# Optimization experiments

Hardware: AMD Instinct MI355X
Metric: run time of the kernel (lower is better)

Reference implementation:

```python
import jax, jax.numpy as jnp
from jax import lax
import numpy as np

NUM_CLASSES = 80
STRIDES = (8, 16, 32)
CONF_THRE = 0.01
NMS_THRE = 0.65
TOPK = 500  # fixed pre-NMS candidate cap (jit-compatible stand-in for dynamic conf filter)


def setup_inputs() -> dict:
    key = jax.random.key(0)
    k8, k16, k32 = jax.random.split(key, 3)
    B, C = 8, 5 + NUM_CLASSES
    return {
        "out8": jax.random.normal(k8, (B, C, 160, 160), dtype=jnp.float32),
        "out16": jax.random.normal(k16, (B, C, 80, 80), dtype=jnp.float32),
        "out32": jax.random.normal(k32, (B, C, 40, 40), dtype=jnp.float32),
    }


def _decode_level(x, stride):
    # x: [B, C, H, W] -> decoded [B, H*W, C]
    B, C, H, W = x.shape
    x = x.reshape(B, C, H * W).transpose(0, 2, 1)  # [B, HW, C]
    yv, xv = jnp.meshgrid(jnp.arange(H), jnp.arange(W), indexing="ij")
    grid = jnp.stack([xv, yv], axis=-1).reshape(1, H * W, 2).astype(x.dtype)
    s = jnp.asarray(stride, x.dtype)
    xy = (x[..., 0:2] + grid) * s
    wh = jnp.exp(x[..., 2:4]) * s
    obj = jax.nn.sigmoid(x[..., 4:5])
    cls = jax.nn.sigmoid(x[..., 5:])
    return jnp.concatenate([xy, wh, obj, cls], axis=-1)


def _iou_one_vs_all(box, boxes):
    # box: [4] xyxy, boxes: [K,4] xyxy
    x1 = jnp.maximum(box[0], boxes[:, 0])
    y1 = jnp.maximum(box[1], boxes[:, 1])
    x2 = jnp.minimum(box[2], boxes[:, 2])
    y2 = jnp.minimum(box[3], boxes[:, 3])
    inter = jnp.maximum(x2 - x1, 0.0) * jnp.maximum(y2 - y1, 0.0)
    a1 = jnp.maximum(box[2] - box[0], 0.0) * jnp.maximum(box[3] - box[1], 0.0)
    a2 = jnp.maximum(boxes[:, 2] - boxes[:, 0], 0.0) * jnp.maximum(boxes[:, 3] - boxes[:, 1], 0.0)
    return inter / (a1 + a2 - inter + 1e-9)


def _nms_keep(boxes, valid, iou_thr):
    # boxes are pre-sorted by descending score; returns bool keep mask [K]
    K = boxes.shape[0]
    idx = jnp.arange(K)

    def body(i, state):
        keep, suppressed = state
        cur_ok = jnp.logical_not(suppressed[i])
        keep = keep.at[i].set(cur_ok)
        iou = _iou_one_vs_all(boxes[i], boxes)
        suppressed = suppressed | ((iou > iou_thr) & cur_ok & (idx > i))
        return keep, suppressed

    keep, _ = lax.fori_loop(0, K, body, (jnp.zeros(K, bool), jnp.logical_not(valid)))
    return keep


def _post_process_image(pred):
    # pred: [N, 5+num_classes] decoded, boxes already xyxy
    cls_scores = pred[:, 5:5 + NUM_CLASSES]
    class_conf = jnp.max(cls_scores, axis=1)
    class_pred = jnp.argmax(cls_scores, axis=1)
    obj = pred[:, 4]
    total = obj * class_conf  # NMS score, same as torchvision call
    masked = jnp.where(total >= CONF_THRE, total, -1.0)
    top_sc, top_i = lax.top_k(masked, TOPK)  # sorted descending
    boxes = pred[top_i, :4]
    obj_k = obj[top_i]
    cc_k = class_conf[top_i]
    lab_k = class_pred[top_i]
    valid = top_sc >= CONF_THRE
    # class-aware (batched) NMS via per-class coordinate offset, as torchvision does
    max_c = jnp.max(jnp.where(valid[:, None], boxes, 0.0)) + 1.0
    boxes_off = boxes + (lab_k.astype(boxes.dtype) * max_c)[:, None]
    keep = _nms_keep(boxes_off, valid, NMS_THRE)
    det = jnp.concatenate(
        [boxes, obj_k[:, None], cc_k[:, None], lab_k.astype(boxes.dtype)[:, None]], axis=1
    )  # [K, 7] = (x1,y1,x2,y2,obj,class_conf,class_id)
    return det * keep[:, None].astype(det.dtype)


def reference(out8, out16, out32):
    levels = [(out8, 8), (out16, 16), (out32, 32)]
    pred = jnp.concatenate([_decode_level(x, s) for x, s in levels], axis=1)  # [B, N, C]
    # cxcywh -> xyxy corners
    cx, cy, w, h = pred[..., 0], pred[..., 1], pred[..., 2], pred[..., 3]
    corners = jnp.stack([cx - w / 2, cy - h / 2, cx + w / 2, cy + h / 2], axis=-1)
    pred = jnp.concatenate([corners, pred[..., 4:]], axis=-1)
    return jax.vmap(_post_process_image)(pred)  # [B, TOPK, 7], zero-padded
```

## Files before the change

kernel.cpp:

```cpp
#include <hip/hip_runtime.h>

#define NPI    33600
#define KTOP   500
#define CAP    1024
#define KEY001 0xBC23D70Au
#define NGRP   1024
#define NIMG   8

__device__ __forceinline__ float sigmoidf_(float x) {
  return 1.0f / (1.0f + expf(-x));
}
__device__ __forceinline__ unsigned fkey(float f) {
  unsigned u = __float_as_uint(f);
  return (u & 0x80000000u) ? ~u : (u | 0x80000000u);
}

__global__ __launch_bounds__(256) void k_decode(
    const float* __restrict__ p8, const float* __restrict__ p16,
    const float* __restrict__ p32,
    unsigned* __restrict__ keys, float* __restrict__ dets,
    unsigned* __restrict__ hist2)
{
  const int b = blockIdx.y;
  const int t = blockIdx.x * 256 + threadIdx.x;
  const int a = t * 4;
  __shared__ unsigned lh[NGRP];
  for (int i = threadIdx.x; i < NGRP; i += 256) lh[i] = 0;
  __syncthreads();

  if (a < NPI) {
    const float* lvl; int j, W, HW, S;
    if (a < 25600)      { lvl = p8;  j = a;         W = 160; HW = 25600; S = 8;  }
    else if (a < 32000) { lvl = p16; j = a - 25600; W = 80;  HW = 6400;  S = 16; }
    else                { lvl = p32; j = a - 32000; W = 40;  HW = 1600;  S = 32; }
    const float* base = lvl + (size_t)b * 85 * HW + j;
    float4 t0 = *(const float4*)(base);
    float4 t1 = *(const float4*)(base + (size_t)1 * HW);
    float4 t2 = *(const float4*)(base + (size_t)2 * HW);
    float4 t3 = *(const float4*)(base + (size_t)3 * HW);
    float4 t4 = *(const float4*)(base + (size_t)4 * HW);
    float cc[4] = {-1.0f, -1.0f, -1.0f, -1.0f};
    int   lab[4] = {0, 0, 0, 0};
    #pragma unroll
    for (int c0 = 0; c0 < 80; c0 += 8) {
      float4 r[8];
      #pragma unroll
      for (int u = 0; u < 8; ++u)
        r[u] = *(const float4*)(base + (size_t)(5 + c0 + u) * HW);
      #pragma unroll
      for (int u = 0; u < 8; ++u) {
        float s;
        s = sigmoidf_(r[u].x); if (s > cc[0]) { cc[0] = s; lab[0] = c0 + u; }
        s = sigmoidf_(r[u].y); if (s > cc[1]) { cc[1] = s; lab[1] = c0 + u; }
        s = sigmoidf_(r[u].z); if (s > cc[2]) { cc[2] = s; lab[2] = c0 + u; }
        s = sigmoidf_(r[u].w); if (s > cc[3]) { cc[3] = s; lab[3] = c0 + u; }
      }
    }
    float e0[4] = {t0.x, t0.y, t0.z, t0.w};
    float e1[4] = {t1.x, t1.y, t1.z, t1.w};
    float e2[4] = {t2.x, t2.y, t2.z, t2.w};
    float e3[4] = {t3.x, t3.y, t3.z, t3.w};
    float e4[4] = {t4.x, t4.y, t4.z, t4.w};
    unsigned k4[4];
    float dv[7][4];
    #pragma unroll
    for (int e = 0; e < 4; ++e) {
      float obj = sigmoidf_(e4[e]);
      float tot = obj * cc[e];
      k4[e] = fkey(tot >= 0.01f ? tot : -1.0f);
      int jj = j + e;
      int gy = jj / W, gx = jj - gy * W;
      float fs = (float)S;
      float cx = (e0[e] + (float)gx) * fs;
      float cy = (e1[e] + (float)gy) * fs;
      float w  = expf(e2[e]) * fs;
      float h  = expf(e3[e]) * fs;
      dv[0][e] = cx - 0.5f * w; dv[1][e] = cy - 0.5f * h;
      dv[2][e] = cx + 0.5f * w; dv[3][e] = cy + 0.5f * h;
      dv[4][e] = obj; dv[5][e] = cc[e]; dv[6][e] = (float)lab[e];
    }
    *(uint4*)(keys + (size_t)b * NPI + a) = make_uint4(k4[0], k4[1], k4[2], k4[3]);
    const size_t P  = (size_t)NIMG * NPI;
    const size_t pa = (size_t)b * NPI + a;
    #pragma unroll
    for (int c = 0; c < 7; ++c)
      *(float4*)(dets + (size_t)c * P + pa) =
          make_float4(dv[c][0], dv[c][1], dv[c][2], dv[c][3]);
    #pragma unroll
    for (int e = 0; e < 4; ++e) atomicAdd(&lh[k4[e] >> 22], 1u);
  }
  __syncthreads();
  unsigned* gb = hist2 + (size_t)b * NGRP;
  for (int i = threadIdx.x; i < NGRP; i += 256) {
    unsigned v = lh[i];
    if (v) atomicAdd(&gb[i], v);
  }
}

__global__ __launch_bounds__(1024) void k_post(
    const unsigned* __restrict__ hist2, const unsigned* __restrict__ keys,
    const float* __restrict__ dets, float* __restrict__ out)
{
  const int b    = blockIdx.x;
  const int tid  = threadIdx.x;
  const int lane = tid & 63;
  const int wave = tid >> 6;

  __shared__ unsigned lh[NGRP];
  __shared__ unsigned sh_sub[4096];
  __shared__ unsigned sh_c64[64];
  __shared__ unsigned sh_G, sh_Chi10, sh_T, sh_Chi, sh_nA, sh_nB;
  __shared__ unsigned long long sh_cand[CAP];
  __shared__ float sh_det[KTOP][7];
  __shared__ float sh_box[KTOP][4];
  __shared__ unsigned sh_mask[KTOP * 16];
  __shared__ unsigned sh_inval[16];
  __shared__ unsigned sh_keep[16];
  __shared__ unsigned sh_wcA[16], sh_wcB[16];
  __shared__ float sh_red[16];
  __shared__ float sh_maxc;

  lh[tid] = hist2[(size_t)b * NGRP + tid];
  for (int i = tid; i < 4096; i += 1024) sh_sub[i] = 0;
  __syncthreads();
  if (tid < 64) {
    unsigned s = 0;
    #pragma unroll
    for (int k = 0; k < 16; ++k) s += lh[tid * 16 + k];
    sh_c64[tid] = s;
  }
  __syncthreads();
  if (tid == 0) {
    unsigned cum = 0; int C = 0;
    for (int g = 63; g >= 0; --g) {
      unsigned v = sh_c64[g];
      if (cum + v >= KTOP) { C = g; break; }
      cum += v;
    }
    int G = C * 16; unsigned chi = cum;
    for (int g = C * 16 + 15; g >= C * 16; --g) {
      unsigned v = lh[g];
      if (chi + v >= KTOP) { G = g; break; }
      chi += v;
    }
    sh_G = (unsigned)G; sh_Chi10 = chi;
    sh_nA = 0; sh_nB = 0;
  }
  __syncthreads();
  const unsigned G = sh_G;
  const unsigned* kb = keys + (size_t)b * NPI;

  for (int i = tid; i < NPI; i += 1024) {
    unsigned k = kb[i];
    if ((k >> 22) == G) atomicAdd(&sh_sub[(k >> 10) & 4095u], 1u);
  }
  __syncthreads();
  if (tid < 64) {
    unsigned s = 0;
    for (int k = 0; k < 64; ++k) s += sh_sub[tid * 64 + k];
    sh_c64[tid] = s;
  }
  __syncthreads();
  if (tid == 0) {
    unsigned c = sh_Chi10; int C2 = 0;
    for (int g = 63; g >= 0; --g) {
      unsigned v = sh_c64[g];
      if (c + v >= KTOP) { C2 = g; break; }
      c += v;
    }
    int T12 = C2 * 64;
    for (int t2 = C2 * 64 + 63; t2 >= C2 * 64; --t2) {
      unsigned v = sh_sub[t2];
      if (c + v >= KTOP) { T12 = t2; break; }
      c += v;
    }
    sh_T = (G << 12) | (unsigned)T12;
    sh_Chi = c;
  }
  __syncthreads();
  const unsigned T = sh_T, Chi = sh_Chi;
  const unsigned Bcap = CAP - Chi;

  for (int chunk = 0; chunk < 9; ++chunk) {
    int a0 = chunk * 4096 + tid * 4;
    unsigned kk[4]; bool iA[4], iB[4];
    bool act = (a0 < NPI);
    if (act) {
      uint4 kv = *(const uint4*)(kb + a0);
      kk[0] = kv.x; kk[1] = kv.y; kk[2] = kv.z; kk[3] = kv.w;
    } else { kk[0] = kk[1] = kk[2] = kk[3] = 0u; }
    #pragma unroll
    for (int e = 0; e < 4; ++e) {
      unsigned bin = kk[e] >> 10;
      iA[e] = act && (bin > T);
      iB[e] = act && (bin == T);
    }
    unsigned long long balA[4], balB[4];
    #pragma unroll
    for (int e = 0; e < 4; ++e) { balA[e] = __ballot(iA[e]); balB[e] = __ballot(iB[e]); }
    if (lane == 0) {
      unsigned sA = 0, sB = 0;
      #pragma unroll
      for (int e = 0; e < 4; ++e) { sA += (unsigned)__popcll(balA[e]); sB += (unsigned)__popcll(balB[e]); }
      sh_wcA[wave] = sA; sh_wcB[wave] = sB;
    }
    __syncthreads();
    unsigned pA = sh_nA, pB = sh_nB;
    for (int w2 = 0; w2 < wave; ++w2) { pA += sh_wcA[w2]; pB += sh_wcB[w2]; }
    unsigned long long lt = (1ULL << lane) - 1ULL;
    #pragma unroll
    for (int e = 0; e < 4; ++e) {
      pA += (unsigned)__popcll(balA[e] & lt);
      pB += (unsigned)__popcll(balB[e] & lt);
    }
    #pragma unroll
    for (int e = 0; e < 4; ++e) {
      unsigned long long packed =
          ((unsigned long long)kk[e] << 32) |
          (unsigned long long)(0xFFFFFFFFu - (unsigned)(a0 + e));
      if (iA[e]) { sh_cand[pA] = packed; ++pA; }
      if (iB[e]) { if (pB < Bcap) sh_cand[CAP - 1 - pB] = packed; ++pB; }
    }
    __syncthreads();
    if (tid == 0) {
      unsigned sA = 0, sB = 0;
      for (int w2 = 0; w2 < 16; ++w2) { sA += sh_wcA[w2]; sB += sh_wcB[w2]; }
      sh_nA += sA; sh_nB += sB;
    }
    __syncthreads();
  }
  {
    const unsigned nA  = sh_nA;
    const unsigned nBk = (sh_nB < Bcap) ? sh_nB : Bcap;
    for (int s = (int)nA + tid; s < (int)(CAP - nBk); s += 1024) sh_cand[s] = 0ULL;
  }
  __syncthreads();

  for (unsigned kk2 = 2; kk2 <= CAP; kk2 <<= 1) {
    for (unsigned jj = kk2 >> 1; jj > 0; jj >>= 1) {
      unsigned i = (unsigned)tid, p = i ^ jj;
      if (p > i) {
        unsigned long long x = sh_cand[i], y = sh_cand[p];
        bool desc = ((i & kk2) == 0);
        if ((x < y) == desc) { sh_cand[i] = y; sh_cand[p] = x; }
      }
      __syncthreads();
    }
  }

  bool validk = false;
  float contrib = -INFINITY;
  if (tid < KTOP) {
    unsigned long long v = sh_cand[tid];
    unsigned keyk = (unsigned)(v >> 32);
    int a = (int)(0xFFFFFFFFu - (unsigned)(v & 0xFFFFFFFFull));
    if (a < 0) a = 0;
    const size_t P  = (size_t)NIMG * NPI;
    const size_t pa = (size_t)b * NPI + (size_t)a;
    float det[7];
    #pragma unroll
    for (int c = 0; c < 7; ++c) det[c] = dets[(size_t)c * P + pa];
    #pragma unroll
    for (int c = 0; c < 7; ++c) sh_det[tid][c] = det[c];
    validk = (keyk >= KEY001);
    float m4 = fmaxf(fmaxf(det[0], det[1]), fmaxf(det[2], det[3]));
    contrib = validk ? m4 : 0.0f;
  }
  float r = contrib;
  #pragma unroll
  for (int off = 32; off > 0; off >>= 1) r = fmaxf(r, __shfl_xor(r, off));
  if (lane == 0) sh_red[wave] = r;
  unsigned long long bv = __ballot((tid < KTOP) && !validk);
  if (wave < 8 && lane == 0) {
    sh_inval[wave * 2]     = (unsigned)(bv & 0xFFFFFFFFull);
    sh_inval[wave * 2 + 1] = (unsigned)(bv >> 32);
  }
  __syncthreads();
  if (tid == 0) {
    float m = -INFINITY;
    for (int w2 = 0; w2 < 16; ++w2) m = fmaxf(m, sh_red[w2]);
    sh_maxc = m + 1.0f;
  }
  __syncthreads();
  const float maxc = sh_maxc;
  if (tid < KTOP) {
    float offb = sh_det[tid][6] * maxc;
    #pragma unroll
    for (int d = 0; d < 4; ++d) sh_box[tid][d] = sh_det[tid][d] + offb;
  }
  __syncthreads();

  for (int task = tid; task < KTOP * 16; task += 1024) {
    int i = task % KTOP;
    int w = task / KTOP;
    int jbase = w * 32;
    unsigned bits = 0u;
    if (jbase + 31 > i) {
      float ix1 = sh_box[i][0], iy1 = sh_box[i][1], ix2 = sh_box[i][2], iy2 = sh_box[i][3];
      float a1 = fmaxf(ix2 - ix1, 0.0f) * fmaxf(iy2 - iy1, 0.0f);
      #pragma unroll 4
      for (int jj = 0; jj < 32; ++jj) {
        int j = jbase + jj;
        if (j < KTOP && j > i) {
          float jx1 = sh_box[j][0], jy1 = sh_box[j][1];
          float jx2 = sh_box[j][2], jy2 = sh_box[j][3];
          float iw = fminf(ix2, jx2) - fmaxf(ix1, jx1);
          float ih = fminf(iy2, jy2) - fmaxf(iy1, jy1);
          float inter = fmaxf(iw, 0.0f) * fmaxf(ih, 0.0f);
          float a2 = fmaxf(jx2 - jx1, 0.0f) * fmaxf(jy2 - jy1, 0.0f);
          if (inter > 0.65f * (a1 + a2 - inter + 1e-9f)) bits |= (1u << jj);
        }
      }
    }
    sh_mask[i * 16 + w] = bits;
  }
  __syncthreads();

  if (tid < 64) {
    unsigned sup   = (lane < 16) ? sh_inval[lane] : 0u;
    unsigned keepw = 0u;
    unsigned cur = (unsigned)__builtin_amdgcn_readlane((int)sup, 0);
    unsigned mA = (lane < 16) ? sh_mask[0 * 16 + lane] : 0u;
    unsigned mB = (lane < 16) ? sh_mask[1 * 16 + lane] : 0u;
    for (int i = 0; i < KTOP; i += 2) {
      bool ok = ((cur >> (i & 31)) & 1u) == 0u;
      if (ok) {
        sup |= mA;
        if (lane == (i >> 5)) keepw |= (1u << (i & 31));
      }
      cur = (unsigned)__builtin_amdgcn_readlane((int)sup, (i + 1) >> 5);
      mA = (lane < 16 && (i + 2) < KTOP) ? sh_mask[(i + 2) * 16 + lane] : 0u;
      bool ok2 = ((cur >> ((i + 1) & 31)) & 1u) == 0u;
      if (ok2) {
        sup |= mB;
        if (lane == ((i + 1) >> 5)) keepw |= (1u << ((i + 1) & 31));
      }
      cur = (unsigned)__builtin_amdgcn_readlane((int)sup, (i + 2) >> 5);
      mB = (lane < 16 && (i + 3) < KTOP) ? sh_mask[(i + 3) * 16 + lane] : 0u;
    }
    if (lane < 16) sh_keep[lane] = keepw;
  }
  __syncthreads();

  for (int x = tid; x < KTOP * 7; x += 1024) {
    int k = x / 7, c = x - k * 7;
    float keepf = ((sh_keep[k >> 5] >> (k & 31)) & 1u) ? 1.0f : 0.0f;
    out[(size_t)b * (KTOP * 7) + x] = sh_det[k][c] * keepf;
  }
}

extern "C" void kernel_launch(void* const* d_in, const int* in_sizes, int n_in,
                              void* d_out, int out_size, void* d_ws, size_t ws_size,
                              hipStream_t stream) {
  const float* p8  = (const float*)d_in[0];
  const float* p16 = (const float*)d_in[1];
  const float* p32 = (const float*)d_in[2];
  float* out = (float*)d_out;
  unsigned* hist2 = (unsigned*)d_ws;
  unsigned* keys  = hist2 + (size_t)NIMG * NGRP;
  float*    dets  = (float*)(keys + (size_t)NIMG * NPI);

  hipMemsetAsync(hist2, 0, (size_t)NIMG * NGRP * 4, stream);
  k_decode<<<dim3(33, NIMG), 256, 0, stream>>>(p8, p16, p32, keys, dets, hist2);
  k_post<<<dim3(NIMG), 1024, 0, stream>>>(hist2, keys, dets, out);
}
```

Baseline: 250.0 us.

## Split post-processing into select, IoU and NMS kernels; retile decode per level

The decode kernel now uses 128-thread blocks that each stay within one pyramid level, and it loads 16 class channels per batch. The single 8-block post kernel is split into three kernels. A selection kernel does two-pass per-wave candidate compaction, which removes the per-chunk block barriers. An IoU kernel spreads the pairwise mask computation over 16x8 blocks using an SoA box layout with precomputed areas. An NMS kernel reads the mask back into padded shared memory. The goal is more parallelism for the IoU stage and fewer barriers during selection, in exchange for two extra launches and global round-trips of the mask and detections.

```diff
diff --git a/kernel.cpp b/kernel.cpp
--- a/kernel.cpp
+++ b/kernel.cpp
@@ -6,6 +6,7 @@
 #define KEY001 0xBC23D70Au
 #define NGRP   1024
 #define NIMG   8
+#define GPW    525
 
 __device__ __forceinline__ float sigmoidf_(float x) {
   return 1.0f / (1.0f + expf(-x));
@@ -15,25 +16,26 @@
   return (u & 0x80000000u) ? ~u : (u | 0x80000000u);
 }
 
-__global__ __launch_bounds__(256) void k_decode(
+__global__ __launch_bounds__(128) void k_decode(
     const float* __restrict__ p8, const float* __restrict__ p16,
     const float* __restrict__ p32,
     unsigned* __restrict__ keys, float* __restrict__ dets,
     unsigned* __restrict__ hist2)
 {
-  const int b = blockIdx.y;
-  const int t = blockIdx.x * 256 + threadIdx.x;
-  const int a = t * 4;
+  const int b  = blockIdx.y;
+  const int tx = blockIdx.x;
+  const float* lvl; int HW, W, S, j0, abase;
+  if (tx < 50)      { lvl = p8;  HW = 25600; W = 160; S = 8;  j0 = tx * 512;        abase = 0; }
+  else if (tx < 63) { lvl = p16; HW = 6400;  W = 80;  S = 16; j0 = (tx - 50) * 512; abase = 25600; }
+  else              { lvl = p32; HW = 1600;  W = 40;  S = 32; j0 = (tx - 63) * 512; abase = 32000; }
   __shared__ unsigned lh[NGRP];
-  for (int i = threadIdx.x; i < NGRP; i += 256) lh[i] = 0;
-  __syncthreads();
-
-  if (a < NPI) {
-    const float* lvl; int j, W, HW, S;
-    if (a < 25600)      { lvl = p8;  j = a;         W = 160; HW = 25600; S = 8;  }
-    else if (a < 32000) { lvl = p16; j = a - 25600; W = 80;  HW = 6400;  S = 16; }
-    else                { lvl = p32; j = a - 32000; W = 40;  HW = 1600;  S = 32; }
-    const float* base = lvl + (size_t)b * 85 * HW + j;
+  for (int i = threadIdx.x; i < NGRP; i += 128) lh[i] = 0;
+  __syncthreads();
+
+  const int e = j0 + 4 * threadIdx.x;
+  const bool act = (e < HW);
+  if (act) {
+    const float* base = lvl + (size_t)b * 85 * HW + e;
     float4 t0 = *(const float4*)(base);
     float4 t1 = *(const float4*)(base + (size_t)1 * HW);
     float4 t2 = *(const float4*)(base + (size_t)2 * HW);
@@ -41,19 +43,18 @@
     float4 t4 = *(const float4*)(base + (size_t)4 * HW);
     float cc[4] = {-1.0f, -1.0f, -1.0f, -1.0f};
     int   lab[4] = {0, 0, 0, 0};
-    #pragma unroll
-    for (int c0 = 0; c0 < 80; c0 += 8) {
-      float4 r[8];
+    for (int c0 = 5; c0 < 85; c0 += 16) {
+      float4 r[16];
       #pragma unroll
-      for (int u = 0; u < 8; ++u)
-        r[u] = *(const float4*)(base + (size_t)(5 + c0 + u) * HW);
+      for (int u = 0; u < 16; ++u)
+        r[u] = *(const float4*)(base + (size_t)(c0 + u) * HW);
       #pragma unroll
-      for (int u = 0; u < 8; ++u) {
+      for (int u = 0; u < 16; ++u) {
         float s;
-        s = sigmoidf_(r[u].x); if (s > cc[0]) { cc[0] = s; lab[0] = c0 + u; }
-        s = sigmoidf_(r[u].y); if (s > cc[1]) { cc[1] = s; lab[1] = c0 + u; }
-        s = sigmoidf_(r[u].z); if (s > cc[2]) { cc[2] = s; lab[2] = c0 + u; }
-        s = sigmoidf_(r[u].w); if (s > cc[3]) { cc[3] = s; lab[3] = c0 + u; }
+        s = sigmoidf_(r[u].x); if (s > cc[0]) { cc[0] = s; lab[0] = c0 + u - 5; }
+        s = sigmoidf_(r[u].y); if (s > cc[1]) { cc[1] = s; lab[1] = c0 + u - 5; }
+        s = sigmoidf_(r[u].z); if (s > cc[2]) { cc[2] = s; lab[2] = c0 + u - 5; }
+        s = sigmoidf_(r[u].w); if (s > cc[3]) { cc[3] = s; lab[3] = c0 + u - 5; }
       }
     }
     float e0[4] = {t0.x, t0.y, t0.z, t0.w};
@@ -64,21 +65,22 @@
     unsigned k4[4];
     float dv[7][4];
     #pragma unroll
-    for (int e = 0; e < 4; ++e) {
-      float obj = sigmoidf_(e4[e]);
-      float tot = obj * cc[e];
-      k4[e] = fkey(tot >= 0.01f ? tot : -1.0f);
-      int jj = j + e;
+    for (int q = 0; q < 4; ++q) {
+      float obj = sigmoidf_(e4[q]);
+      float tot = obj * cc[q];
+      k4[q] = fkey(tot >= 0.01f ? tot : -1.0f);
+      int jj = e + q;
       int gy = jj / W, gx = jj - gy * W;
       float fs = (float)S;
-      float cx = (e0[e] + (float)gx) * fs;
-      float cy = (e1[e] + (float)gy) * fs;
-      float w  = expf(e2[e]) * fs;
-      float h  = expf(e3[e]) * fs;
-      dv[0][e] = cx - 0.5f * w; dv[1][e] = cy - 0.5f * h;
-      dv[2][e] = cx + 0.5f * w; dv[3][e] = cy + 0.5f * h;
-      dv[4][e] = obj; dv[5][e] = cc[e]; dv[6][e] = (float)lab[e];
-    }
+      float cx = (e0[q] + (float)gx) * fs;
+      float cy = (e1[q] + (float)gy) * fs;
+      float w  = expf(e2[q]) * fs;
+      float h  = expf(e3[q]) * fs;
+      dv[0][q] = cx - 0.5f * w; dv[1][q] = cy - 0.5f * h;
+      dv[2][q] = cx + 0.5f * w; dv[3][q] = cy + 0.5f * h;
+      dv[4][q] = obj; dv[5][q] = cc[q]; dv[6][q] = (float)lab[q];
+    }
+    const int a = abase + e;
     *(uint4*)(keys + (size_t)b * NPI + a) = make_uint4(k4[0], k4[1], k4[2], k4[3]);
     const size_t P  = (size_t)NIMG * NPI;
     const size_t pa = (size_t)b * NPI + a;
@@ -87,19 +89,21 @@
       *(float4*)(dets + (size_t)c * P + pa) =
           make_float4(dv[c][0], dv[c][1], dv[c][2], dv[c][3]);
     #pragma unroll
-    for (int e = 0; e < 4; ++e) atomicAdd(&lh[k4[e] >> 22], 1u);
+    for (int q = 0; q < 4; ++q) atomicAdd(&lh[k4[q] >> 22], 1u);
   }
   __syncthreads();
   unsigned* gb = hist2 + (size_t)b * NGRP;
-  for (int i = threadIdx.x; i < NGRP; i += 256) {
+  for (int i = threadIdx.x; i < NGRP; i += 128) {
     unsigned v = lh[i];
     if (v) atomicAdd(&gb[i], v);
   }
 }
 
-__global__ __launch_bounds__(1024) void k_post(
+__global__ __launch_bounds__(1024) void k_select(
     const unsigned* __restrict__ hist2, const unsigned* __restrict__ keys,
-    const float* __restrict__ dets, float* __restrict__ out)
+    const float* __restrict__ dets,
+    float* __restrict__ topdet, float* __restrict__ soa,
+    unsigned* __restrict__ invalg)
 {
   const int b    = blockIdx.x;
   const int tid  = threadIdx.x;
@@ -109,13 +113,10 @@
   __shared__ unsigned lh[NGRP];
   __shared__ unsigned sh_sub[4096];
   __shared__ unsigned sh_c64[64];
-  __shared__ unsigned sh_G, sh_Chi10, sh_T, sh_Chi, sh_nA, sh_nB;
-  __shared__ unsigned long long sh_cand[CAP];
+  __shared__ unsigned sh_G, sh_T;
+  __shared__ __align__(16) unsigned long long sh_cand[CAP];
   __shared__ float sh_det[KTOP][7];
-  __shared__ float sh_box[KTOP][4];
-  __shared__ unsigned sh_mask[KTOP * 16];
   __shared__ unsigned sh_inval[16];
-  __shared__ unsigned sh_keep[16];
   __shared__ unsigned sh_wcA[16], sh_wcB[16];
   __shared__ float sh_red[16];
   __shared__ float sh_maxc;
@@ -143,17 +144,22 @@
       if (chi + v >= KTOP) { G = g; break; }
       chi += v;
     }
-    sh_G = (unsigned)G; sh_Chi10 = chi;
-    sh_nA = 0; sh_nB = 0;
+    sh_G = (unsigned)G;
+    sh_c64[0] = chi;
   }
   __syncthreads();
   const unsigned G = sh_G;
   const unsigned* kb = keys + (size_t)b * NPI;
 
-  for (int i = tid; i < NPI; i += 1024) {
-    unsigned k = kb[i];
-    if ((k >> 22) == G) atomicAdd(&sh_sub[(k >> 10) & 4095u], 1u);
-  }
+  for (int g = tid; g < NPI / 4; g += 1024) {
+    uint4 kv = ((const uint4*)kb)[g];
+    unsigned kk[4] = {kv.x, kv.y, kv.z, kv.w};
+    #pragma unroll
+    for (int q = 0; q < 4; ++q)
+      if ((kk[q] >> 22) == G) atomicAdd(&sh_sub[(kk[q] >> 10) & 4095u], 1u);
+  }
+  __syncthreads();
+  unsigned chi10 = sh_c64[0];
   __syncthreads();
   if (tid < 64) {
     unsigned s = 0;
@@ -162,7 +168,7 @@
   }
   __syncthreads();
   if (tid == 0) {
-    unsigned c = sh_Chi10; int C2 = 0;
+    unsigned c = chi10; int C2 = 0;
     for (int g = 63; g >= 0; --g) {
       unsigned v = sh_c64[g];
       if (c + v >= KTOP) { C2 = g; break; }
@@ -175,65 +181,74 @@
       c += v;
     }
     sh_T = (G << 12) | (unsigned)T12;
-    sh_Chi = c;
-  }
-  __syncthreads();
-  const unsigned T = sh_T, Chi = sh_Chi;
-  const unsigned Bcap = CAP - Chi;
-
-  for (int chunk = 0; chunk < 9; ++chunk) {
-    int a0 = chunk * 4096 + tid * 4;
-    unsigned kk[4]; bool iA[4], iB[4];
-    bool act = (a0 < NPI);
-    if (act) {
-      uint4 kv = *(const uint4*)(kb + a0);
-      kk[0] = kv.x; kk[1] = kv.y; kk[2] = kv.z; kk[3] = kv.w;
-    } else { kk[0] = kk[1] = kk[2] = kk[3] = 0u; }
-    #pragma unroll
-    for (int e = 0; e < 4; ++e) {
-      unsigned bin = kk[e] >> 10;
-      iA[e] = act && (bin > T);
-      iB[e] = act && (bin == T);
-    }
+  }
+  __syncthreads();
+  const unsigned T = sh_T;
+
+  unsigned runA = 0, runB = 0;
+  for (int it = 0; it < 9; ++it) {
+    int gl = it * 64 + lane;
+    bool act = (gl < GPW);
+    int g = wave * GPW + gl;
+    uint4 kv = act ? ((const uint4*)kb)[g] : make_uint4(0, 0, 0, 0);
+    unsigned kk[4] = {kv.x, kv.y, kv.z, kv.w};
+    #pragma unroll
+    for (int q = 0; q < 4; ++q) {
+      unsigned bin = kk[q] >> 10;
+      runA += (unsigned)__popcll(__ballot(act && (bin > T)));
+      runB += (unsigned)__popcll(__ballot(act && (bin == T)));
+    }
+  }
+  if (lane == 0) { sh_wcA[wave] = runA; sh_wcB[wave] = runB; }
+  __syncthreads();
+  unsigned pA = 0, pB = 0, nA = 0, nBtot = 0;
+  #pragma unroll
+  for (int w2 = 0; w2 < 16; ++w2) {
+    unsigned va = sh_wcA[w2], vb = sh_wcB[w2];
+    if (w2 < wave) { pA += va; pB += vb; }
+    nA += va; nBtot += vb;
+  }
+  const unsigned Bcap = CAP - nA;
+  const unsigned nBk  = (nBtot < Bcap) ? nBtot : Bcap;
+  const int nTot = (int)(nA + nBk);
+
+  for (int it = 0; it < 9; ++it) {
+    int gl = it * 64 + lane;
+    bool act = (gl < GPW);
+    int g = wave * GPW + gl;
+    uint4 kv = act ? ((const uint4*)kb)[g] : make_uint4(0, 0, 0, 0);
+    unsigned kk[4] = {kv.x, kv.y, kv.z, kv.w};
+    bool iA[4], iB[4];
     unsigned long long balA[4], balB[4];
     #pragma unroll
-    for (int e = 0; e < 4; ++e) { balA[e] = __ballot(iA[e]); balB[e] = __ballot(iB[e]); }
-    if (lane == 0) {
-      unsigned sA = 0, sB = 0;
-      #pragma unroll
-      for (int e = 0; e < 4; ++e) { sA += (unsigned)__popcll(balA[e]); sB += (unsigned)__popcll(balB[e]); }
-      sh_wcA[wave] = sA; sh_wcB[wave] = sB;
-    }
-    __syncthreads();
-    unsigned pA = sh_nA, pB = sh_nB;
-    for (int w2 = 0; w2 < wave; ++w2) { pA += sh_wcA[w2]; pB += sh_wcB[w2]; }
+    for (int q = 0; q < 4; ++q) {
+      unsigned bin = kk[q] >> 10;
+      iA[q] = act && (bin > T);
+      iB[q] = act && (bin == T);
+      balA[q] = __ballot(iA[q]);
+      balB[q] = __ballot(iB[q]);
+    }
     unsigned long long lt = (1ULL << lane) - 1ULL;
-    #pragma unroll
-    for (int e = 0; e < 4; ++e) {
-      pA += (unsigned)__popcll(balA[e] & lt);
-      pB += (unsigned)__popcll(balB[e] & lt);
-    }
-    #pragma unroll
-    for (int e = 0; e < 4; ++e) {
+    unsigned pAl = pA, pBl = pB;
+    #pragma unroll
+    for (int q = 0; q < 4; ++q) {
+      pAl += (unsigned)__popcll(balA[q] & lt);
+      pBl += (unsigned)__popcll(balB[q] & lt);
+    }
+    #pragma unroll
+    for (int q = 0; q < 4; ++q) {
+      int a0 = g * 4 + q;
       unsigned long long packed =
-          ((unsigned long long)kk[e] << 32) |
-          (unsigned long long)(0xFFFFFFFFu - (unsigned)(a0 + e));
-      if (iA[e]) { sh_cand[pA] = packed; ++pA; }
-      if (iB[e]) { if (pB < Bcap) sh_cand[CAP - 1 - pB] = packed; ++pB; }
-    }
-    __syncthreads();
-    if (tid == 0) {
-      unsigned sA = 0, sB = 0;
-      for (int w2 = 0; w2 < 16; ++w2) { sA += sh_wcA[w2]; sB += sh_wcB[w2]; }
-      sh_nA += sA; sh_nB += sB;
-    }
-    __syncthreads();
-  }
-  {
-    const unsigned nA  = sh_nA;
-    const unsigned nBk = (sh_nB < Bcap) ? sh_nB : Bcap;
-    for (int s = (int)nA + tid; s < (int)(CAP - nBk); s += 1024) sh_cand[s] = 0ULL;
-  }
+          ((unsigned long long)kk[q] << 32) |
+          (unsigned long long)(0xFFFFFFFFu - (unsigned)a0);
+      if (iA[q]) { sh_cand[pAl] = packed; ++pAl; }
+      if (iB[q]) { if (pBl < Bcap) sh_cand[nA + pBl] = packed; ++pBl; }
+      pA += (unsigned)__popcll(balA[q]);
+      pB += (unsigned)__popcll(balB[q]);
+    }
+  }
+  __syncthreads();
+  for (int s = nTot + tid; s < CAP; s += 1024) sh_cand[s] = 0ULL;
   __syncthreads();
 
   for (unsigned kk2 = 2; kk2 <= CAP; kk2 <<= 1) {
@@ -250,6 +265,7 @@
 
   bool validk = false;
   float contrib = -INFINITY;
+  float det[7] = {0, 0, 0, 0, 0, 0, 0};
   if (tid < KTOP) {
     unsigned long long v = sh_cand[tid];
     unsigned keyk = (unsigned)(v >> 32);
@@ -257,7 +273,6 @@
     if (a < 0) a = 0;
     const size_t P  = (size_t)NIMG * NPI;
     const size_t pa = (size_t)b * NPI + (size_t)a;
-    float det[7];
     #pragma unroll
     for (int c = 0; c < 7; ++c) det[c] = dets[(size_t)c * P + pa];
     #pragma unroll
@@ -283,45 +298,83 @@
   }
   __syncthreads();
   const float maxc = sh_maxc;
-  if (tid < KTOP) {
-    float offb = sh_det[tid][6] * maxc;
-    #pragma unroll
-    for (int d = 0; d < 4; ++d) sh_box[tid][d] = sh_det[tid][d] + offb;
-  }
-  __syncthreads();
-
-  for (int task = tid; task < KTOP * 16; task += 1024) {
-    int i = task % KTOP;
-    int w = task / KTOP;
-    int jbase = w * 32;
+  if (tid < 512) {
+    float x1, y1, x2, y2, ar;
+    if (tid < KTOP) {
+      float offb = det[6] * maxc;
+      x1 = det[0] + offb; y1 = det[1] + offb;
+      x2 = det[2] + offb; y2 = det[3] + offb;
+      ar = fmaxf(x2 - x1, 0.0f) * fmaxf(y2 - y1, 0.0f);
+    } else { x1 = y1 = x2 = y2 = ar = 0.0f; }
+    soa[(0 * NIMG + b) * 512 + tid] = x1;
+    soa[(1 * NIMG + b) * 512 + tid] = y1;
+    soa[(2 * NIMG + b) * 512 + tid] = x2;
+    soa[(3 * NIMG + b) * 512 + tid] = y2;
+    soa[(4 * NIMG + b) * 512 + tid] = ar;
+  }
+  if (tid < 16) invalg[b * 16 + tid] = sh_inval[tid];
+  for (int x = tid; x < KTOP * 7; x += 1024)
+    topdet[(size_t)b * (KTOP * 7) + x] = ((const float*)sh_det)[x];
+}
+
+__global__ __launch_bounds__(256) void k_iou(
+    const float* __restrict__ soa, unsigned* __restrict__ gmask)
+{
+  const int w = blockIdx.x, b = blockIdx.y;
+  const int tid = threadIdx.x;
+  __shared__ float sx1[512], sy1[512], sx2[512], sy2[512], sa[512];
+  for (int x = tid; x < 512; x += 256) {
+    sx1[x] = soa[(0 * NIMG + b) * 512 + x];
+    sy1[x] = soa[(1 * NIMG + b) * 512 + x];
+    sx2[x] = soa[(2 * NIMG + b) * 512 + x];
+    sy2[x] = soa[(3 * NIMG + b) * 512 + x];
+    sa[x]  = soa[(4 * NIMG + b) * 512 + x];
+  }
+  __syncthreads();
+  const int jbase = w * 32;
+  for (int i = tid; i < KTOP; i += 256) {
     unsigned bits = 0u;
     if (jbase + 31 > i) {
-      float ix1 = sh_box[i][0], iy1 = sh_box[i][1], ix2 = sh_box[i][2], iy2 = sh_box[i][3];
-      float a1 = fmaxf(ix2 - ix1, 0.0f) * fmaxf(iy2 - iy1, 0.0f);
+      float ix1 = sx1[i], iy1 = sy1[i], ix2 = sx2[i], iy2 = sy2[i];
+      float a1 = sa[i];
       #pragma unroll 4
       for (int jj = 0; jj < 32; ++jj) {
         int j = jbase + jj;
         if (j < KTOP && j > i) {
-          float jx1 = sh_box[j][0], jy1 = sh_box[j][1];
-          float jx2 = sh_box[j][2], jy2 = sh_box[j][3];
+          float jx1 = sx1[j], jy1 = sy1[j];
+          float jx2 = sx2[j], jy2 = sy2[j];
+          float a2  = sa[j];
           float iw = fminf(ix2, jx2) - fmaxf(ix1, jx1);
           float ih = fminf(iy2, jy2) - fmaxf(iy1, jy1);
           float inter = fmaxf(iw, 0.0f) * fmaxf(ih, 0.0f);
-          float a2 = fmaxf(jx2 - jx1, 0.0f) * fmaxf(jy2 - jy1, 0.0f);
           if (inter > 0.65f * (a1 + a2 - inter + 1e-9f)) bits |= (1u << jj);
         }
       }
     }
-    sh_mask[i * 16 + w] = bits;
-  }
-  __syncthreads();
-
+    gmask[((size_t)b * 16 + w) * 512 + i] = bits;
+  }
+}
+
+__global__ __launch_bounds__(256) void k_nms(
+    const unsigned* __restrict__ gmask, const unsigned* __restrict__ invalg,
+    const float* __restrict__ topdet, float* __restrict__ out)
+{
+  const int b = blockIdx.x;
+  const int tid = threadIdx.x;
+  const int lane = tid & 63;
+  __shared__ unsigned sm[KTOP * 17];
+  __shared__ unsigned sh_keep[16];
+  for (int g = tid; g < KTOP * 16; g += 256) {
+    int w = g / KTOP, i = g - w * KTOP;
+    sm[i * 17 + w] = gmask[((size_t)b * 16 + w) * 512 + i];
+  }
+  __syncthreads();
   if (tid < 64) {
-    unsigned sup   = (lane < 16) ? sh_inval[lane] : 0u;
+    unsigned sup   = (lane < 16) ? invalg[b * 16 + lane] : 0u;
     unsigned keepw = 0u;
     unsigned cur = (unsigned)__builtin_amdgcn_readlane((int)sup, 0);
-    unsigned mA = (lane < 16) ? sh_mask[0 * 16 + lane] : 0u;
-    unsigned mB = (lane < 16) ? sh_mask[1 * 16 + lane] : 0u;
+    unsigned mA = (lane < 16) ? sm[0 * 17 + lane] : 0u;
+    unsigned mB = (lane < 16) ? sm[1 * 17 + lane] : 0u;
     for (int i = 0; i < KTOP; i += 2) {
       bool ok = ((cur >> (i & 31)) & 1u) == 0u;
       if (ok) {
@@ -329,23 +382,22 @@
         if (lane == (i >> 5)) keepw |= (1u << (i & 31));
       }
       cur = (unsigned)__builtin_amdgcn_readlane((int)sup, (i + 1) >> 5);
-      mA = (lane < 16 && (i + 2) < KTOP) ? sh_mask[(i + 2) * 16 + lane] : 0u;
+      mA = (lane < 16 && (i + 2) < KTOP) ? sm[(i + 2) * 17 + lane] : 0u;
       bool ok2 = ((cur >> ((i + 1) & 31)) & 1u) == 0u;
       if (ok2) {
         sup |= mB;
         if (lane == ((i + 1) >> 5)) keepw |= (1u << ((i + 1) & 31));
       }
       cur = (unsigned)__builtin_amdgcn_readlane((int)sup, (i + 2) >> 5);
-      mB = (lane < 16 && (i + 3) < KTOP) ? sh_mask[(i + 3) * 16 + lane] : 0u;
+      mB = (lane < 16 && (i + 3) < KTOP) ? sm[(i + 3) * 17 + lane] : 0u;
     }
     if (lane < 16) sh_keep[lane] = keepw;
   }
   __syncthreads();
-
-  for (int x = tid; x < KTOP * 7; x += 1024) {
-    int k = x / 7, c = x - k * 7;
+  for (int x = tid; x < KTOP * 7; x += 256) {
+    int k = x / 7;
     float keepf = ((sh_keep[k >> 5] >> (k & 31)) & 1u) ? 1.0f : 0.0f;
-    out[(size_t)b * (KTOP * 7) + x] = sh_det[k][c] * keepf;
+    out[(size_t)b * (KTOP * 7) + x] = topdet[(size_t)b * (KTOP * 7) + x] * keepf;
   }
 }
 
@@ -356,11 +408,17 @@
   const float* p16 = (const float*)d_in[1];
   const float* p32 = (const float*)d_in[2];
   float* out = (float*)d_out;
-  unsigned* hist2 = (unsigned*)d_ws;
-  unsigned* keys  = hist2 + (size_t)NIMG * NGRP;
-  float*    dets  = (float*)(keys + (size_t)NIMG * NPI);
+  unsigned* hist2  = (unsigned*)d_ws;
+  unsigned* keys   = hist2 + (size_t)NIMG * NGRP;
+  float*    dets   = (float*)(keys + (size_t)NIMG * NPI);
+  float*    topdet = dets + (size_t)7 * NIMG * NPI;
+  float*    soa    = topdet + (size_t)NIMG * KTOP * 7;
+  unsigned* invalg = (unsigned*)(soa + (size_t)5 * NIMG * 512);
+  unsigned* gmask  = invalg + NIMG * 16;
 
   hipMemsetAsync(hist2, 0, (size_t)NIMG * NGRP * 4, stream);
-  k_decode<<<dim3(33, NIMG), 256, 0, stream>>>(p8, p16, p32, keys, dets, hist2);
-  k_post<<<dim3(NIMG), 1024, 0, stream>>>(hist2, keys, dets, out);
-}
+  k_decode<<<dim3(67, NIMG), 128, 0, stream>>>(p8, p16, p32, keys, dets, hist2);
+  k_select<<<dim3(NIMG), 1024, 0, stream>>>(hist2, keys, dets, topdet, soa, invalg);
+  k_iou<<<dim3(16, NIMG), 256, 0, stream>>>(soa, gmask);
+  k_nms<<<dim3(NIMG), 256, 0, stream>>>(gmask, invalg, topdet, out);
+}
```

After: 210.0 us. -16.0%, faster.
